# Kernel optimization log

Hardware: AMD Instinct MI355X
Metric: run time of the kernel (lower is better)

Reference implementation:

```python
import jax, jax.numpy as jnp
import numpy as np

EMBED_DIM = 512
NUM_HEADS = 8
EDGE_THRESHOLD = 0.1


def setup_inputs() -> dict:
    key = jax.random.key(0)
    ks = jax.random.split(key, 8)
    E, H = EMBED_DIM, NUM_HEADS
    B, S = 2, 2048
    s = 0.02
    return {
        'hidden_states': jax.random.normal(ks[0], (B, S, E), jnp.float32),
        'Wq': jax.random.normal(ks[1], (E, E), jnp.float32) * s,
        'bq': jnp.zeros((E,), jnp.float32),
        'Wk': jax.random.normal(ks[2], (E, E), jnp.float32) * s,
        'bk': jnp.zeros((E,), jnp.float32),
        'Wv': jax.random.normal(ks[3], (E, E), jnp.float32) * s,
        'bv': jnp.zeros((E,), jnp.float32),
        'Wm1': jax.random.normal(ks[4], (E, E + H), jnp.float32) * s,
        'bm1': jnp.zeros((E,), jnp.float32),
        'Wm2': jax.random.normal(ks[5], (E, E), jnp.float32) * s,
        'bm2': jnp.zeros((E,), jnp.float32),
        'Wo': jax.random.normal(ks[6], (E, E), jnp.float32) * s,
        'bo': jnp.zeros((E,), jnp.float32),
    }


def reference(hidden_states, Wq, bq, Wk, bk, Wv, bv, Wm1, bm1, Wm2, bm2, Wo, bo):
    B, S, E = hidden_states.shape
    H = NUM_HEADS
    hd = E // H
    scale = 1.0 / np.sqrt(hd).astype(np.float32)
    x = hidden_states

    q = (x @ Wq.T + bq).reshape(B, S, H, hd)
    k = (x @ Wk.T + bk).reshape(B, S, H, hd)
    v = (x @ Wv.T + bv)  # kept flat [B,S,E]

    # edge weights: softmax over source nodes j, per head
    scores = jnp.einsum('bihd,bjhd->bijh', q, k) * scale  # [B,S,S,H]
    edge_weights = jax.nn.softmax(scores, axis=2)
    ew_mean = edge_weights.mean(axis=-1)  # [B,S,S]
    adjacency = (ew_mean > EDGE_THRESHOLD).astype(x.dtype)

    # message passing: mean of (edge-weighted features) over adjacent neighbors
    masked_w = ew_mean * adjacency
    aggregated = jnp.einsum('bij,bjd->bid', masked_w, x)
    num_neighbors = jnp.clip(adjacency.sum(axis=-1, keepdims=True), 1.0, None)
    messages = aggregated / num_neighbors

    # gated MLP over [node_features ; mean edge features]
    edge_features = edge_weights.mean(axis=2)  # [B,S,H]
    combined = jnp.concatenate([x, edge_features], axis=-1)
    h = jax.nn.gelu(combined @ Wm1.T + bm1, approximate=False)
    updated = (h @ Wm2.T + bm2) + messages

    attended = jnp.einsum('bij,bjd->bid', ew_mean, v)
    out = (updated + attended) @ Wo.T + bo  # dropout p=0 -> identity
    return out
```

## Files before the change

### kernel.cpp

```cpp
#include <hip/hip_runtime.h>
#include <hip/hip_bf16.h>
#include <math.h>

#define BB 2
#define SS 2048
#define EE 512
#define HH 8
#define NN (BB*SS)
#define JC1 8
#define JCP 4

typedef __attribute__((ext_vector_type(8))) short short8;
typedef __attribute__((ext_vector_type(4))) float f32x4;

__device__ __forceinline__ float b2f(short v){
    return __uint_as_float(((unsigned)(unsigned short)v) << 16);
}
__device__ __forceinline__ unsigned f2bf(float f){
    unsigned u = __float_as_uint(f);
    u += 0x7fffu + ((u >> 16) & 1u);
    return u >> 16;
}
__device__ __forceinline__ void stage16_f32(const float* __restrict__ src,
                                            __hip_bfloat16* dst){
    const float4 f0 = *reinterpret_cast<const float4*>(src);
    const float4 f1 = *reinterpret_cast<const float4*>(src + 4);
    const float4 f2 = *reinterpret_cast<const float4*>(src + 8);
    const float4 f3 = *reinterpret_cast<const float4*>(src + 12);
    uint4 o0, o1;
    o0.x = f2bf(f0.x) | (f2bf(f0.y) << 16);
    o0.y = f2bf(f0.z) | (f2bf(f0.w) << 16);
    o0.z = f2bf(f1.x) | (f2bf(f1.y) << 16);
    o0.w = f2bf(f1.z) | (f2bf(f1.w) << 16);
    o1.x = f2bf(f2.x) | (f2bf(f2.y) << 16);
    o1.y = f2bf(f2.z) | (f2bf(f2.w) << 16);
    o1.z = f2bf(f3.x) | (f2bf(f3.y) << 16);
    o1.w = f2bf(f3.z) | (f2bf(f3.w) << 16);
    *reinterpret_cast<uint4*>(dst) = o0;
    *reinterpret_cast<uint4*>(dst + 8) = o1;
}
__device__ __forceinline__ void stage16_b16(const __hip_bfloat16* __restrict__ src,
                                            __hip_bfloat16* dst){
    const uint4* s = reinterpret_cast<const uint4*>(src);
    uint4* d = reinterpret_cast<uint4*>(dst);
    d[0] = s[0]; d[1] = s[1];
}

__global__ void conv_bf16(
    const float* s0, const float* s1, const float* s2, const float* s3,
    const float* s4, const float* s5, const float* s6,
    __hip_bfloat16* d0, __hip_bfloat16* d1, __hip_bfloat16* d2, __hip_bfloat16* d3,
    __hip_bfloat16* d4, __hip_bfloat16* d5, __hip_bfloat16* d6)
{
    const int which = blockIdx.y;
    const float* s; __hip_bfloat16* d; int n;
    switch (which) {
        case 0: s = s0; d = d0; n = 2097152; break;
        case 1: s = s1; d = d1; n = 262144; break;
        case 2: s = s2; d = d2; n = 262144; break;
        case 3: s = s3; d = d3; n = 262144; break;
        case 4: s = s4; d = d4; n = 266240; break;
        case 5: s = s5; d = d5; n = 262144; break;
        default: s = s6; d = d6; n = 262144; break;
    }
    const int base = (blockIdx.x * 256 + threadIdx.x) * 4;
    if (base >= n) return;
    const float4 f = *reinterpret_cast<const float4*>(s + base);
    uint2 o;
    o.x = f2bf(f.x) | (f2bf(f.y) << 16);
    o.y = f2bf(f.z) | (f2bf(f.w) << 16);
    *reinterpret_cast<uint2*>(d + base) = o;
}

template<int B16>
__global__ __launch_bounds__(256) void qkv_gemm(
    const void* __restrict__ x,
    const void* __restrict__ Wq, const float* __restrict__ bq,
    const void* __restrict__ Wk, const float* __restrict__ bk,
    const void* __restrict__ Wv, const float* __restrict__ bv,
    __hip_bfloat16* __restrict__ qb,
    __hip_bfloat16* __restrict__ kb,
    __hip_bfloat16* __restrict__ vT)
{
    __shared__ __hip_bfloat16 As[64][72];
    __shared__ __hip_bfloat16 Bs[64][72];
    const int tid = threadIdx.x;
    const int which = blockIdx.x >> 3;
    const int col0 = (blockIdx.x & 7) * 64;
    const int row0 = blockIdx.y * 64;
    const int wv = tid >> 6, lane = tid & 63, quad = lane >> 4, m16 = lane & 15;
    const int sr = tid >> 2;
    const int sc = (tid & 3) * 16;
    const void* W    = (which == 0) ? Wq : (which == 1) ? Wk : Wv;
    const float* bias = (which == 0) ? bq : (which == 1) ? bk : bv;

    f32x4 acc[4];
    #pragma unroll
    for (int nt = 0; nt < 4; ++nt) acc[nt] = (f32x4){0.f, 0.f, 0.f, 0.f};

    for (int k0 = 0; k0 < 512; k0 += 64) {
        if (B16) {
            stage16_b16((const __hip_bfloat16*)x + (size_t)(row0 + sr) * EE + k0 + sc, &As[sr][sc]);
            stage16_b16((const __hip_bfloat16*)W + (size_t)(col0 + sr) * EE + k0 + sc, &Bs[sr][sc]);
        } else {
            stage16_f32((const float*)x + (size_t)(row0 + sr) * EE + k0 + sc, &As[sr][sc]);
            stage16_f32((const float*)W + (size_t)(col0 + sr) * EE + k0 + sc, &Bs[sr][sc]);
        }
        __syncthreads();
        #pragma unroll
        for (int ks = 0; ks < 2; ++ks) {
            const short8 a = *reinterpret_cast<const short8*>(
                &As[wv * 16 + m16][ks * 32 + quad * 8]);
            #pragma unroll
            for (int nt = 0; nt < 4; ++nt) {
                const short8 b = *reinterpret_cast<const short8*>(
                    &Bs[nt * 16 + m16][ks * 32 + quad * 8]);
                acc[nt] = __builtin_amdgcn_mfma_f32_16x16x32_bf16(a, b, acc[nt], 0, 0, 0);
            }
        }
        __syncthreads();
    }

    if (which == 2) {
        #pragma unroll
        for (int nt = 0; nt < 4; ++nt) {
            const float bb = bias[col0 + nt * 16 + m16];
            #pragma unroll
            for (int r = 0; r < 4; ++r)
                Bs[wv * 16 + quad * 4 + r][nt * 16 + m16] =
                    __float2bfloat16(acc[nt][r] + bb);
        }
        __syncthreads();
        const int bb2 = row0 >> 11;
        const int j0 = row0 & (SS - 1);
        const int er = tid >> 2;
        const int js = (tid & 3) * 16;
        unsigned pk[8];
        #pragma unroll
        for (int p = 0; p < 8; ++p) {
            const unsigned lo = *reinterpret_cast<const unsigned short*>(&Bs[js + 2*p][er]);
            const unsigned hi = *reinterpret_cast<const unsigned short*>(&Bs[js + 2*p + 1][er]);
            pk[p] = lo | (hi << 16);
        }
        uint4 s0; s0.x = pk[0]; s0.y = pk[1]; s0.z = pk[2]; s0.w = pk[3];
        uint4 s1; s1.x = pk[4]; s1.y = pk[5]; s1.z = pk[6]; s1.w = pk[7];
        __hip_bfloat16* dst = vT + ((size_t)(bb2 * EE + col0 + er)) * SS + j0 + js;
        *reinterpret_cast<uint4*>(dst) = s0;
        *reinterpret_cast<uint4*>(dst + 8) = s1;
    } else {
        __hip_bfloat16* C = (which == 0) ? qb : kb;
        #pragma unroll
        for (int nt = 0; nt < 4; ++nt) {
            const int gn = col0 + nt * 16 + m16;
            const float bb = bias[gn];
            #pragma unroll
            for (int r = 0; r < 4; ++r) {
                const int gm = row0 + wv * 16 + quad * 4 + r;
                C[(size_t)gm * EE + gn] = __float2bfloat16(acc[nt][r] + bb);
            }
        }
    }
}

template<int MODE, int AB16, int WB16, int CF32>
__global__ __launch_bounds__(256) void gemm_bt(
    const void* __restrict__ Av,
    const void* __restrict__ Wv_,
    const float* __restrict__ bias,
    void* __restrict__ Cv,
    int ldb)
{
    __shared__ __hip_bfloat16 As[64][72];
    __shared__ __hip_bfloat16 Bs[64][72];
    const int tid = threadIdx.x;
    const int col0 = blockIdx.x * 64;
    const int row0 = blockIdx.y * 64;
    const int wv = tid >> 6, lane = tid & 63, quad = lane >> 4, m16 = lane & 15;
    const int sr = tid >> 2;
    const int sc = (tid & 3) * 16;

    f32x4 acc[4];
    #pragma unroll
    for (int nt = 0; nt < 4; ++nt) acc[nt] = (f32x4){0.f, 0.f, 0.f, 0.f};

    for (int k0 = 0; k0 < 512; k0 += 64) {
        if (AB16)
            stage16_b16((const __hip_bfloat16*)Av + (size_t)(row0 + sr) * EE + k0 + sc, &As[sr][sc]);
        else
            stage16_f32((const float*)Av + (size_t)(row0 + sr) * EE + k0 + sc, &As[sr][sc]);
        if (WB16)
            stage16_b16((const __hip_bfloat16*)Wv_ + (size_t)(col0 + sr) * ldb + k0 + sc, &Bs[sr][sc]);
        else
            stage16_f32((const float*)Wv_ + (size_t)(col0 + sr) * ldb + k0 + sc, &Bs[sr][sc]);
        __syncthreads();
        #pragma unroll
        for (int ks = 0; ks < 2; ++ks) {
            const short8 a = *reinterpret_cast<const short8*>(
                &As[wv * 16 + m16][ks * 32 + quad * 8]);
            #pragma unroll
            for (int nt = 0; nt < 4; ++nt) {
                const short8 b = *reinterpret_cast<const short8*>(
                    &Bs[nt * 16 + m16][ks * 32 + quad * 8]);
                acc[nt] = __builtin_amdgcn_mfma_f32_16x16x32_bf16(a, b, acc[nt], 0, 0, 0);
            }
        }
        __syncthreads();
    }

    #pragma unroll
    for (int nt = 0; nt < 4; ++nt) {
        const int gn = col0 + nt * 16 + m16;
        float bb = bias[gn];
        if (MODE == 1) {
            float ts = 0.f;
            #pragma unroll
            for (int h = 0; h < 8; ++h) {
                const size_t wi = (size_t)gn * ldb + 512 + h;
                ts += WB16 ? (float)((const __hip_bfloat16*)Wv_)[wi]
                           : ((const float*)Wv_)[wi];
            }
            bb += ts * (1.0f / (float)SS);
        }
        #pragma unroll
        for (int r = 0; r < 4; ++r) {
            const int gm = row0 + wv * 16 + quad * 4 + r;
            const size_t ci = (size_t)gm * EE + gn;
            float c = acc[nt][r] + bb;
            if (MODE == 1) c = 0.5f * c * (1.0f + erff(c * 0.70710678118654752f));
            if (MODE == 2) c += (float)((const __hip_bfloat16*)Cv)[ci];
            if (CF32) ((float*)Cv)[ci] = c;
            else      ((__hip_bfloat16*)Cv)[ci] = __float2bfloat16(c);
        }
    }
}

__global__ __launch_bounds__(256) void attn_denoms(
    const __hip_bfloat16* __restrict__ qws,
    const __hip_bfloat16* __restrict__ kws,
    float* __restrict__ dnP,
    int* __restrict__ cntI)
{
    __shared__ __hip_bfloat16 KL[2][16][520];
    const int tid = threadIdx.x;
    const int wv = tid >> 6, lane = tid & 63, quad = lane >> 4, m16 = lane & 15;
    const int jc = blockIdx.x;
    const int it = blockIdx.y;
    const int b  = blockIdx.z;
    const size_t g0 = (size_t)b * SS + it * 32;
    const size_t gb = (size_t)b * SS;
    const int ih = wv & 1, hh = wv >> 1;

    if (jc == 0 && tid < 32) cntI[g0 + tid] = 0;

    short8 aq[4][2];
    #pragma unroll
    for (int hp = 0; hp < 4; ++hp)
        #pragma unroll
        for (int ks = 0; ks < 2; ++ks)
            aq[hp][ks] = *reinterpret_cast<const short8*>(
                qws + (g0 + ih * 16 + m16) * EE + (hh * 4 + hp) * 64 + ks * 32 + quad * 8);

    float dph[4][4];
    #pragma unroll
    for (int hp = 0; hp < 4; ++hp)
        #pragma unroll
        for (int r = 0; r < 4; ++r) dph[hp][r] = 0.f;

    const int srow = tid >> 4, t4 = tid & 15;
    {
        #pragma unroll
        for (int k = 0; k < 4; ++k)
            *reinterpret_cast<uint4*>(&KL[0][srow][t4 * 8 + k * 128]) =
                *reinterpret_cast<const uint4*>(
                    kws + (gb + jc * 256 + srow) * EE + t4 * 8 + k * 128);
    }

    for (int jt = 0; jt < 16; ++jt) {
        __syncthreads();
        uint4 kr[4];
        if (jt + 1 < 16) {
            #pragma unroll
            for (int k = 0; k < 4; ++k)
                kr[k] = *reinterpret_cast<const uint4*>(
                    kws + (gb + jc * 256 + (jt + 1) * 16 + srow) * EE + t4 * 8 + k * 128);
        }
        #pragma unroll
        for (int hp = 0; hp < 4; ++hp) {
            const short8 b0 = *reinterpret_cast<const short8*>(
                &KL[jt & 1][m16][(hh * 4 + hp) * 64 + quad * 8]);
            const short8 b1 = *reinterpret_cast<const short8*>(
                &KL[jt & 1][m16][(hh * 4 + hp) * 64 + 32 + quad * 8]);
            f32x4 c = {0.f, 0.f, 0.f, 0.f};
            c = __builtin_amdgcn_mfma_f32_16x16x32_bf16(aq[hp][0], b0, c, 0, 0, 0);
            c = __builtin_amdgcn_mfma_f32_16x16x32_bf16(aq[hp][1], b1, c, 0, 0, 0);
            #pragma unroll
            for (int r = 0; r < 4; ++r) dph[hp][r] += __expf(c[r] * 0.125f);
        }
        if (jt + 1 < 16) {
            #pragma unroll
            for (int k = 0; k < 4; ++k)
                *reinterpret_cast<uint4*>(&KL[(jt + 1) & 1][srow][t4 * 8 + k * 128]) = kr[k];
        }
    }

    #pragma unroll
    for (int hp = 0; hp < 4; ++hp)
        #pragma unroll
        for (int off = 1; off <= 8; off <<= 1)
            #pragma unroll
            for (int r = 0; r < 4; ++r) dph[hp][r] += __shfl_xor(dph[hp][r], off, 64);
    if (m16 == 0) {
        const size_t i = (size_t)it * 32 + ih * 16 + quad * 4;
        #pragma unroll
        for (int hp = 0; hp < 4; ++hp)
            #pragma unroll
            for (int r = 0; r < 4; ++r)
                dnP[((size_t)(jc * BB + b) * SS + i + r) * HH + hh * 4 + hp] = dph[hp][r];
    }
}

__global__ __launch_bounds__(256, 2) void attn_ewpv(
    const __hip_bfloat16* __restrict__ qws,
    const __hip_bfloat16* __restrict__ kws,
    const __hip_bfloat16* __restrict__ vTg,
    const float* __restrict__ dnP,
    int* __restrict__ cntI,
    int* __restrict__ slotJ,
    float* __restrict__ slotW,
    __hip_bfloat16* __restrict__ pvP)
{
    __shared__ __hip_bfloat16 KL[32][520];
    __shared__ __hip_bfloat16 ewT[32][40];
    __shared__ float invd[HH][32];
    const int tid = threadIdx.x;
    const int wv = tid >> 6, lane = tid & 63, quad = lane >> 4, m16 = lane & 15;
    const int jc = blockIdx.x;
    const int it = blockIdx.y;
    const int b  = blockIdx.z;
    const size_t gb = (size_t)b * SS;
    const size_t g0 = gb + it * 32;
    const int ih = wv & 1;
    const int jh = wv >> 1;

    {
        const int h = tid >> 5, i = tid & 31;
        float s = 0.f;
        #pragma unroll
        for (int c = 0; c < JC1; ++c)
            s += dnP[((size_t)(c * BB + b) * SS + it * 32 + i) * HH + h];
        invd[h][i] = 0.125f / s;
    }

    short8 aq[HH][2];
    #pragma unroll
    for (int h = 0; h < HH; ++h)
        #pragma unroll
        for (int ks = 0; ks < 2; ++ks)
            aq[h][ks] = *reinterpret_cast<const short8*>(
                qws + (g0 + ih * 16 + m16) * EE + h * 64 + ks * 32 + quad * 8);

    f32x4 acc[2][8];
    #pragma unroll
    for (int mf = 0; mf < 2; ++mf)
        #pragma unroll
        for (int nf = 0; nf < 8; ++nf) acc[mf][nf] = (f32x4){0.f, 0.f, 0.f, 0.f};

    const int krow = tid >> 4, kcol = (tid & 15) * 32;
    const __hip_bfloat16* vrow0 = vTg + ((size_t)b * EE + wv * 128 + m16) * SS + quad * 8;

    for (int st = 0; st < 16; ++st) {
        const int j0 = jc * 512 + st * 32;
        #pragma unroll
        for (int rr = 0; rr < 2; ++rr) {
            const uint4* src = reinterpret_cast<const uint4*>(
                kws + (gb + j0 + rr * 16 + krow) * EE + kcol);
            uint4* dst = reinterpret_cast<uint4*>(&KL[rr * 16 + krow][kcol]);
            dst[0] = src[0]; dst[1] = src[1]; dst[2] = src[2]; dst[3] = src[3];
        }
        __syncthreads();

        float wsum[4] = {0.f, 0.f, 0.f, 0.f};
        #pragma unroll
        for (int h = 0; h < HH; ++h) {
            const short8 b0 = *reinterpret_cast<const short8*>(
                &KL[jh * 16 + m16][h * 64 + quad * 8]);
            const short8 b1 = *reinterpret_cast<const short8*>(
                &KL[jh * 16 + m16][h * 64 + 32 + quad * 8]);
            f32x4 c = {0.f, 0.f, 0.f, 0.f};
            c = __builtin_amdgcn_mfma_f32_16x16x32_bf16(aq[h][0], b0, c, 0, 0, 0);
            c = __builtin_amdgcn_mfma_f32_16x16x32_bf16(aq[h][1], b1, c, 0, 0, 0);
            #pragma unroll
            for (int r = 0; r < 4; ++r)
                wsum[r] += __expf(c[r] * 0.125f) * invd[h][ih * 16 + quad * 4 + r];
        }
        #pragma unroll
        for (int r = 0; r < 4; ++r) {
            const __hip_bfloat16 wb = __float2bfloat16(wsum[r]);
            ewT[ih * 16 + quad * 4 + r][jh * 16 + m16] = wb;
            if ((float)wb > 0.1f) {
                const int li = ih * 16 + quad * 4 + r;
                const int idx = atomicAdd(&cntI[g0 + li], 1);
                if (idx < 16) {
                    slotJ[((size_t)g0 + li) * 16 + idx] = j0 + jh * 16 + m16;
                    slotW[((size_t)g0 + li) * 16 + idx] = (float)wb;
                }
            }
        }
        __syncthreads();

        {
            short8 vb[8];
            #pragma unroll
            for (int nf = 0; nf < 8; ++nf)
                vb[nf] = *reinterpret_cast<const short8*>(vrow0 + (size_t)(nf * 16) * SS + j0);
            const short8 a0 = *reinterpret_cast<const short8*>(&ewT[m16][quad * 8]);
            const short8 a1 = *reinterpret_cast<const short8*>(&ewT[16 + m16][quad * 8]);
            #pragma unroll
            for (int nf = 0; nf < 8; ++nf) {
                acc[0][nf] = __builtin_amdgcn_mfma_f32_16x16x32_bf16(a0, vb[nf], acc[0][nf], 0, 0, 0);
                acc[1][nf] = __builtin_amdgcn_mfma_f32_16x16x32_bf16(a1, vb[nf], acc[1][nf], 0, 0, 0);
            }
        }
    }

    #pragma unroll
    for (int mf = 0; mf < 2; ++mf)
        #pragma unroll
        for (int nf = 0; nf < 8; ++nf)
            #pragma unroll
            for (int r = 0; r < 4; ++r)
                KL[mf * 16 + quad * 4 + r][wv * 128 + nf * 16 + m16] =
                    __float2bfloat16(acc[mf][nf][r]);
    __syncthreads();
    const int orow = tid >> 3;
    const int oc = (tid & 7) * 64;
    const uint4* s = reinterpret_cast<const uint4*>(&KL[orow][oc]);
    uint4* d = reinterpret_cast<uint4*>(
        pvP + ((size_t)jc * NN + g0 + orow) * EE + oc);
    #pragma unroll
    for (int q = 0; q < 8; ++q) d[q] = s[q];
}

__global__ __launch_bounds__(256) void pv_combine(
    const __hip_bfloat16* __restrict__ pvP,
    const int* __restrict__ cntI,
    const int* __restrict__ slotJ,
    const float* __restrict__ slotW,
    const float* __restrict__ x,
    __hip_bfloat16* __restrict__ u1out)
{
    const int tid = threadIdx.x;
    const int row = blockIdx.x * 4 + (tid >> 6);
    const int e0 = (tid & 63) * 8;
    float s[8] = {0.f, 0.f, 0.f, 0.f, 0.f, 0.f, 0.f, 0.f};
    #pragma unroll
    for (int c = 0; c < JCP; ++c) {
        const short8 v = *reinterpret_cast<const short8*>(
            pvP + ((size_t)c * NN + row) * EE + e0);
        #pragma unroll
        for (int k = 0; k < 8; ++k) s[k] += b2f(v[k]);
    }
    const int cn = cntI[row];
    if (cn > 0) {
        const float inv = 1.f / (float)cn;
        const int ns = cn < 16 ? cn : 16;
        const int b = row >> 11;
        for (int t = 0; t < ns; ++t) {
            const int j = slotJ[(size_t)row * 16 + t];
            const float w = slotW[(size_t)row * 16 + t] * inv;
            const float* xr = x + ((size_t)b * SS + j) * EE + e0;
            #pragma unroll
            for (int k = 0; k < 8; ++k) s[k] += w * xr[k];
        }
    }
    short8 o;
    #pragma unroll
    for (int k = 0; k < 8; ++k) o[k] = (short)f2bf(s[k]);
    *reinterpret_cast<short8*>(u1out + (size_t)row * EE + e0) = o;
}

extern "C" void kernel_launch(void* const* d_in, const int* in_sizes, int n_in,
                              void* d_out, int out_size, void* d_ws, size_t ws_size,
                              hipStream_t stream)
{
    const float* x   = (const float*)d_in[0];
    const float* Wq  = (const float*)d_in[1];
    const float* bq  = (const float*)d_in[2];
    const float* Wk  = (const float*)d_in[3];
    const float* bk  = (const float*)d_in[4];
    const float* Wv  = (const float*)d_in[5];
    const float* bv  = (const float*)d_in[6];
    const float* Wm1 = (const float*)d_in[7];
    const float* bm1 = (const float*)d_in[8];
    const float* Wm2 = (const float*)d_in[9];
    const float* bm2 = (const float*)d_in[10];
    const float* Wo  = (const float*)d_in[11];
    const float* bo  = (const float*)d_in[12];

    char* ws = (char*)d_ws;
    const size_t MB = 1024 * 1024;
    __hip_bfloat16* qb = (__hip_bfloat16*)(ws + 0);
    __hip_bfloat16* kb = (__hip_bfloat16*)(ws + 4*MB);
    __hip_bfloat16* vT = (__hip_bfloat16*)(ws + 8*MB);
    __hip_bfloat16* pvP = (__hip_bfloat16*)(ws + 12*MB);
    float* dnP = (float*)(ws + 28*MB);
    int*   cntI = (int*)(ws + 29*MB);
    int*   slotJ = (int*)(ws + 29*MB + 64*1024);
    float* slotW = (float*)(ws + 29*MB + 384*1024);
    const bool EXT = (ws_size >= 38 * MB);
    __hip_bfloat16* xb   = (__hip_bfloat16*)(ws + 30*MB);
    __hip_bfloat16* wqb  = (__hip_bfloat16*)(ws + 34*MB);
    __hip_bfloat16* wkb  = (__hip_bfloat16*)(ws + 34*MB + 512*1024);
    __hip_bfloat16* wvb  = (__hip_bfloat16*)(ws + 35*MB);
    __hip_bfloat16* wm1b = (__hip_bfloat16*)(ws + 35*MB + 512*1024);
    __hip_bfloat16* wm2b = (__hip_bfloat16*)(ws + 36*MB + 256*1024);
    __hip_bfloat16* wob  = (__hip_bfloat16*)(ws + 36*MB + 768*1024);

    dim3 blk(256, 1, 1);
    dim3 gg(EE / 64, NN / 64, 1);

    if (EXT) {
        conv_bf16<<<dim3(2048, 7, 1), blk, 0, stream>>>(
            x, Wq, Wk, Wv, Wm1, Wm2, Wo, xb, wqb, wkb, wvb, wm1b, wm2b, wob);
        qkv_gemm<1><<<dim3(24, NN / 64, 1), blk, 0, stream>>>(
            xb, wqb, bq, wkb, bk, wvb, bv, qb, kb, vT);
    } else {
        qkv_gemm<0><<<dim3(24, NN / 64, 1), blk, 0, stream>>>(
            x, Wq, bq, Wk, bk, Wv, bv, qb, kb, vT);
    }
    attn_denoms<<<dim3(JC1, SS / 32, BB), blk, 0, stream>>>(qb, kb, dnP, cntI);
    attn_ewpv<<<dim3(JCP, SS / 32, BB), blk, 0, stream>>>(
        qb, kb, vT, dnP, cntI, slotJ, slotW, pvP);
    pv_combine<<<dim3(NN / 4, 1, 1), blk, 0, stream>>>(
        pvP, cntI, slotJ, slotW, x, qb);
    if (EXT) {
        gemm_bt<1,1,1,0><<<gg, blk, 0, stream>>>(xb, wm1b, bm1, kb, EE + HH);
        gemm_bt<2,1,1,0><<<gg, blk, 0, stream>>>(kb, wm2b, bm2, qb, EE);
        gemm_bt<0,1,1,1><<<gg, blk, 0, stream>>>(qb, wob, bo, d_out, EE);
    } else {
        gemm_bt<1,0,0,0><<<gg, blk, 0, stream>>>(x, Wm1, bm1, kb, EE + HH);
        gemm_bt<2,1,0,0><<<gg, blk, 0, stream>>>(kb, Wm2, bm2, qb, EE);
        gemm_bt<0,1,0,1><<<gg, blk, 0, stream>>>(qb, Wo, bo, d_out, EE);
    }
}
```

Measured before the change: 222.0 us.

## Fuse pv_combine into Wm2 GEMM epilogue and double-buffer GEMM smem tiles

Removes the separate pv_combine kernel. Its partial-sum reduction and sparse neighbour-message accumulation now run in the epilogue of the MODE 2 GEMM, which saves one launch and a round trip of the intermediate through global memory. The gemm_bt main loop also gains double-buffered shared memory: the next K tile is loaded into registers while MFMAs run on the current tile, which drops one barrier per iteration. The trade-offs are more shared memory and registers, and an epilogue that reads with a column-strided, less coalesced pattern.

```diff
diff --git a/kernel.cpp b/kernel.cpp
--- a/kernel.cpp
+++ b/kernel.cpp
@@ -44,6 +44,19 @@
     const uint4* s = reinterpret_cast<const uint4*>(src);
     uint4* d = reinterpret_cast<uint4*>(dst);
     d[0] = s[0]; d[1] = s[1];
+}
+__device__ __forceinline__ void pack16(const float4* f, __hip_bfloat16* dst){
+    uint4 o0, o1;
+    o0.x = f2bf(f[0].x) | (f2bf(f[0].y) << 16);
+    o0.y = f2bf(f[0].z) | (f2bf(f[0].w) << 16);
+    o0.z = f2bf(f[1].x) | (f2bf(f[1].y) << 16);
+    o0.w = f2bf(f[1].z) | (f2bf(f[1].w) << 16);
+    o1.x = f2bf(f[2].x) | (f2bf(f[2].y) << 16);
+    o1.y = f2bf(f[2].z) | (f2bf(f[2].w) << 16);
+    o1.z = f2bf(f[3].x) | (f2bf(f[3].y) << 16);
+    o1.w = f2bf(f[3].z) | (f2bf(f[3].w) << 16);
+    *reinterpret_cast<uint4*>(dst) = o0;
+    *reinterpret_cast<uint4*>(dst + 8) = o1;
 }
 
 __global__ void conv_bf16(
@@ -168,10 +181,15 @@
     const void* __restrict__ Wv_,
     const float* __restrict__ bias,
     void* __restrict__ Cv,
-    int ldb)
+    int ldb,
+    const __hip_bfloat16* __restrict__ pvPp,
+    const int* __restrict__ cntIp,
+    const int* __restrict__ slotJp,
+    const float* __restrict__ slotWp,
+    const float* __restrict__ xf)
 {
-    __shared__ __hip_bfloat16 As[64][72];
-    __shared__ __hip_bfloat16 Bs[64][72];
+    __shared__ __hip_bfloat16 As[2][64][72];
+    __shared__ __hip_bfloat16 Bs[2][64][72];
     const int tid = threadIdx.x;
     const int col0 = blockIdx.x * 64;
     const int row0 = blockIdx.y * 64;
@@ -183,28 +201,95 @@
     #pragma unroll
     for (int nt = 0; nt < 4; ++nt) acc[nt] = (f32x4){0.f, 0.f, 0.f, 0.f};
 
-    for (int k0 = 0; k0 < 512; k0 += 64) {
+    {
         if (AB16)
-            stage16_b16((const __hip_bfloat16*)Av + (size_t)(row0 + sr) * EE + k0 + sc, &As[sr][sc]);
+            stage16_b16((const __hip_bfloat16*)Av + (size_t)(row0 + sr) * EE + sc, &As[0][sr][sc]);
         else
-            stage16_f32((const float*)Av + (size_t)(row0 + sr) * EE + k0 + sc, &As[sr][sc]);
+            stage16_f32((const float*)Av + (size_t)(row0 + sr) * EE + sc, &As[0][sr][sc]);
         if (WB16)
-            stage16_b16((const __hip_bfloat16*)Wv_ + (size_t)(col0 + sr) * ldb + k0 + sc, &Bs[sr][sc]);
+            stage16_b16((const __hip_bfloat16*)Wv_ + (size_t)(col0 + sr) * ldb + sc, &Bs[0][sr][sc]);
         else
-            stage16_f32((const float*)Wv_ + (size_t)(col0 + sr) * ldb + k0 + sc, &Bs[sr][sc]);
-        __syncthreads();
+            stage16_f32((const float*)Wv_ + (size_t)(col0 + sr) * ldb + sc, &Bs[0][sr][sc]);
+    }
+
+    for (int kt = 0; kt < 8; ++kt) {
+        __syncthreads();
+        uint4 ra[2], rb[2];
+        float4 fa[4], fb[4];
+        if (kt + 1 < 8) {
+            const int k0 = (kt + 1) * 64;
+            if (AB16) {
+                const uint4* s = reinterpret_cast<const uint4*>(
+                    (const __hip_bfloat16*)Av + (size_t)(row0 + sr) * EE + k0 + sc);
+                ra[0] = s[0]; ra[1] = s[1];
+            } else {
+                const float4* s = reinterpret_cast<const float4*>(
+                    (const float*)Av + (size_t)(row0 + sr) * EE + k0 + sc);
+                fa[0] = s[0]; fa[1] = s[1]; fa[2] = s[2]; fa[3] = s[3];
+            }
+            if (WB16) {
+                const uint4* s = reinterpret_cast<const uint4*>(
+                    (const __hip_bfloat16*)Wv_ + (size_t)(col0 + sr) * ldb + k0 + sc);
+                rb[0] = s[0]; rb[1] = s[1];
+            } else {
+                const float4* s = reinterpret_cast<const float4*>(
+                    (const float*)Wv_ + (size_t)(col0 + sr) * ldb + k0 + sc);
+                fb[0] = s[0]; fb[1] = s[1]; fb[2] = s[2]; fb[3] = s[3];
+            }
+        }
+        const int cur = kt & 1;
         #pragma unroll
         for (int ks = 0; ks < 2; ++ks) {
             const short8 a = *reinterpret_cast<const short8*>(
-                &As[wv * 16 + m16][ks * 32 + quad * 8]);
+                &As[cur][wv * 16 + m16][ks * 32 + quad * 8]);
             #pragma unroll
             for (int nt = 0; nt < 4; ++nt) {
                 const short8 b = *reinterpret_cast<const short8*>(
-                    &Bs[nt * 16 + m16][ks * 32 + quad * 8]);
+                    &Bs[cur][nt * 16 + m16][ks * 32 + quad * 8]);
                 acc[nt] = __builtin_amdgcn_mfma_f32_16x16x32_bf16(a, b, acc[nt], 0, 0, 0);
             }
         }
-        __syncthreads();
+        if (kt + 1 < 8) {
+            const int nb = (kt + 1) & 1;
+            if (AB16) {
+                uint4* d = reinterpret_cast<uint4*>(&As[nb][sr][sc]);
+                d[0] = ra[0]; d[1] = ra[1];
+            } else pack16(fa, &As[nb][sr][sc]);
+            if (WB16) {
+                uint4* d = reinterpret_cast<uint4*>(&Bs[nb][sr][sc]);
+                d[0] = rb[0]; d[1] = rb[1];
+            } else pack16(fb, &Bs[nb][sr][sc]);
+        }
+    }
+
+    if (MODE == 2) {
+        #pragma unroll
+        for (int r = 0; r < 4; ++r) {
+            const int gm = row0 + wv * 16 + quad * 4 + r;
+            const int cn = cntIp[gm];
+            const int bloc = gm >> 11;
+            #pragma unroll
+            for (int nt = 0; nt < 4; ++nt) {
+                const int gn = col0 + nt * 16 + m16;
+                const size_t ci = (size_t)gm * EE + gn;
+                float c = acc[nt][r] + bias[gn];
+                #pragma unroll
+                for (int cc = 0; cc < JCP; ++cc)
+                    c += b2f(reinterpret_cast<const short*>(pvPp)
+                             [(size_t)cc * NN * EE + ci]);
+                if (cn > 0) {
+                    const float inv = 1.f / (float)cn;
+                    const int ns = cn < 16 ? cn : 16;
+                    for (int t = 0; t < ns; ++t) {
+                        const int j = slotJp[(size_t)gm * 16 + t];
+                        c += slotWp[(size_t)gm * 16 + t] * inv *
+                             xf[((size_t)bloc * SS + j) * EE + gn];
+                    }
+                }
+                ((__hip_bfloat16*)Cv)[ci] = __float2bfloat16(c);
+            }
+        }
+        return;
     }
 
     #pragma unroll
@@ -227,7 +312,6 @@
             const size_t ci = (size_t)gm * EE + gn;
             float c = acc[nt][r] + bb;
             if (MODE == 1) c = 0.5f * c * (1.0f + erff(c * 0.70710678118654752f));
-            if (MODE == 2) c += (float)((const __hip_bfloat16*)Cv)[ci];
             if (CF32) ((float*)Cv)[ci] = c;
             else      ((__hip_bfloat16*)Cv)[ci] = __float2bfloat16(c);
         }
@@ -441,44 +525,6 @@
     for (int q = 0; q < 8; ++q) d[q] = s[q];
 }
 
-__global__ __launch_bounds__(256) void pv_combine(
-    const __hip_bfloat16* __restrict__ pvP,
-    const int* __restrict__ cntI,
-    const int* __restrict__ slotJ,
-    const float* __restrict__ slotW,
-    const float* __restrict__ x,
-    __hip_bfloat16* __restrict__ u1out)
-{
-    const int tid = threadIdx.x;
-    const int row = blockIdx.x * 4 + (tid >> 6);
-    const int e0 = (tid & 63) * 8;
-    float s[8] = {0.f, 0.f, 0.f, 0.f, 0.f, 0.f, 0.f, 0.f};
-    #pragma unroll
-    for (int c = 0; c < JCP; ++c) {
-        const short8 v = *reinterpret_cast<const short8*>(
-            pvP + ((size_t)c * NN + row) * EE + e0);
-        #pragma unroll
-        for (int k = 0; k < 8; ++k) s[k] += b2f(v[k]);
-    }
-    const int cn = cntI[row];
-    if (cn > 0) {
-        const float inv = 1.f / (float)cn;
-        const int ns = cn < 16 ? cn : 16;
-        const int b = row >> 11;
-        for (int t = 0; t < ns; ++t) {
-            const int j = slotJ[(size_t)row * 16 + t];
-            const float w = slotW[(size_t)row * 16 + t] * inv;
-            const float* xr = x + ((size_t)b * SS + j) * EE + e0;
-            #pragma unroll
-            for (int k = 0; k < 8; ++k) s[k] += w * xr[k];
-        }
-    }
-    short8 o;
-    #pragma unroll
-    for (int k = 0; k < 8; ++k) o[k] = (short)f2bf(s[k]);
-    *reinterpret_cast<short8*>(u1out + (size_t)row * EE + e0) = o;
-}
-
 extern "C" void kernel_launch(void* const* d_in, const int* in_sizes, int n_in,
                               void* d_out, int out_size, void* d_ws, size_t ws_size,
                               hipStream_t stream)
@@ -531,15 +577,19 @@
     attn_denoms<<<dim3(JC1, SS / 32, BB), blk, 0, stream>>>(qb, kb, dnP, cntI);
     attn_ewpv<<<dim3(JCP, SS / 32, BB), blk, 0, stream>>>(
         qb, kb, vT, dnP, cntI, slotJ, slotW, pvP);
-    pv_combine<<<dim3(NN / 4, 1, 1), blk, 0, stream>>>(
-        pvP, cntI, slotJ, slotW, x, qb);
     if (EXT) {
-        gemm_bt<1,1,1,0><<<gg, blk, 0, stream>>>(xb, wm1b, bm1, kb, EE + HH);
-        gemm_bt<2,1,1,0><<<gg, blk, 0, stream>>>(kb, wm2b, bm2, qb, EE);
-        gemm_bt<0,1,1,1><<<gg, blk, 0, stream>>>(qb, wob, bo, d_out, EE);
+        gemm_bt<1,1,1,0><<<gg, blk, 0, stream>>>(xb, wm1b, bm1, kb, EE + HH,
+            nullptr, nullptr, nullptr, nullptr, nullptr);
+        gemm_bt<2,1,1,0><<<gg, blk, 0, stream>>>(kb, wm2b, bm2, qb, EE,
+            pvP, cntI, slotJ, slotW, x);
+        gemm_bt<0,1,1,1><<<gg, blk, 0, stream>>>(qb, wob, bo, d_out, EE,
+            nullptr, nullptr, nullptr, nullptr, nullptr);
     } else {
-        gemm_bt<1,0,0,0><<<gg, blk, 0, stream>>>(x, Wm1, bm1, kb, EE + HH);
-        gemm_bt<2,1,0,0><<<gg, blk, 0, stream>>>(kb, Wm2, bm2, qb, EE);
-        gemm_bt<0,1,0,1><<<gg, blk, 0, stream>>>(qb, Wo, bo, d_out, EE);
-    }
-}
+        gemm_bt<1,0,0,0><<<gg, blk, 0, stream>>>(x, Wm1, bm1, kb, EE + HH,
+            nullptr, nullptr, nullptr, nullptr, nullptr);
+        gemm_bt<2,1,0,0><<<gg, blk, 0, stream>>>(kb, Wm2, bm2, qb, EE,
+            pvP, cntI, slotJ, slotW, x);
+        gemm_bt<0,1,0,1><<<gg, blk, 0, stream>>>(qb, Wo, bo, d_out, EE,
+            nullptr, nullptr, nullptr, nullptr, nullptr);
+    }
+}
```

Measured after the change: 219.8 us. Within noise of the previous version (-1.0%).
